# Kernel optimization log

Measured on AMD Instinct MI355X. Metric: run time of the kernel, lower is better.

The kernel has to match this reference:

```python
import jax, jax.numpy as jnp
import numpy as np

EPS = 1e-5


def setup_inputs() -> dict:
    key = jax.random.key(0)
    k1, k2, k3 = jax.random.split(key, 3)
    B, D, T = 16, 256, 4096
    K = 2048
    x = jax.random.normal(k1, (B, D, T), dtype=jnp.float32)
    embedding_sum = jax.random.normal(k2, (K, D), dtype=jnp.float32)
    cluster_usage = jax.random.uniform(k3, (K,), dtype=jnp.float32)
    return {"x": x, "embedding_sum": embedding_sum, "cluster_usage": cluster_usage}


def reference(x, embedding_sum, cluster_usage):
    # embedding property: embedding_sum / clamp(cluster_usage, min=eps)
    emb = embedding_sum / jnp.clip(cluster_usage, EPS, None)[:, None]  # [K, D]
    B, D, T = x.shape
    x_flat = jnp.transpose(x, (0, 2, 1)).reshape(B * T, D)  # (b t) d
    # compute faithfully (clamped for numerical safety).
    x2 = jnp.sum(x_flat * x_flat, axis=-1, keepdims=True)      # [BT, 1]
    e2 = jnp.sum(emb * emb, axis=-1)                           # [K]
    d2 = x2 - 2.0 * (x_flat @ emb.T) + e2[None, :]             # [BT, K]
    distances = jnp.sqrt(jnp.clip(d2, 0.0, None))
    codes = jnp.argmin(distances, axis=-1).reshape(B, 1, T)    # int codes
    # decode: embedding gather, b t d -> b d t
    decoded = jnp.transpose(emb[codes[:, 0, :]], (0, 2, 1))    # [B, D, T]
    return codes, decoded
```

## Files before the change

kernel.cpp:

```cpp
#include <hip/hip_runtime.h>
#include <hip/hip_fp16.h>
#include <cmath>

#define EPS 1e-5f
#define TAU 0.15f
#define RP  8

#define Bn 16
#define Dn 256
#define Tn 4096
#define Kn 2048

typedef unsigned short ushort_t;
typedef __attribute__((ext_vector_type(8))) _Float16 f16x8;
typedef __attribute__((ext_vector_type(4))) float f32x4;

__device__ __forceinline__ unsigned short f2h(float v) {
    return __half_as_ushort(__float2half_rn(v));
}

#define GLOAD_LDS16(gp, lp) __builtin_amdgcn_global_load_lds( \
    (const __attribute__((address_space(1))) unsigned int*)(gp), \
    (__attribute__((address_space(3))) unsigned int*)(lp), 16, 0, 0)

__global__ __launch_bounds__(256) void prep_kernel(
    const float* __restrict__ es, const float* __restrict__ usage,
    float* __restrict__ emb, ushort_t* __restrict__ e16,
    float* __restrict__ bias, float4* __restrict__ embT4,
    int* __restrict__ counter)
{
    __shared__ float sh[256];
    __shared__ float wsum[4];
    const int k = blockIdx.x;
    const int d = threadIdx.x;
    const float inv = 1.0f / fmaxf(usage[k], EPS);
    const float v = es[(size_t)k * Dn + d] * inv;
    emb[(size_t)k * Dn + d] = v;
    e16[(size_t)k * Dn + d] = f2h(fminf(fmaxf(v, -65504.f), 65504.f));
    sh[d] = v;
    float sq = v * v;
    #pragma unroll
    for (int off = 32; off > 0; off >>= 1) sq += __shfl_down(sq, off, 64);
    const int lane = d & 63, wv = d >> 6;
    if (lane == 0) wsum[wv] = sq;
    __syncthreads();
    if (d < 64)
        embT4[(size_t)d * Kn + k] = make_float4(sh[4*d], sh[4*d+1], sh[4*d+2], sh[4*d+3]);
    if (d == 0) {
        bias[k] = 0.5f * (wsum[0] + wsum[1] + wsum[2] + wsum[3]);
        if (k == 0) *counter = 0;
    }
}

__global__ __launch_bounds__(256) void xsplit_kernel(
    const float* __restrict__ x, ushort_t* __restrict__ xh)
{
    __shared__ float tile[32 * 65];
    const int t0 = blockIdx.x * 64;
    const int d0 = blockIdx.y * 32;
    const int b  = blockIdx.z;
    const int tid = threadIdx.x;

    {
        const int dl = tid >> 3, tq = tid & 7;
        const float* src = x + ((size_t)(b * Dn + d0 + dl)) * Tn + t0 + tq * 8;
        const float4 a = *(const float4*)(src);
        const float4 c = *(const float4*)(src + 4);
        float* row = &tile[dl * 65 + tq * 8];
        row[0] = a.x; row[1] = a.y; row[2] = a.z; row[3] = a.w;
        row[4] = c.x; row[5] = c.y; row[6] = c.z; row[7] = c.w;
    }
    __syncthreads();
    {
        const int t_l = tid >> 2, dq = tid & 3;
        unsigned wh[4];
        #pragma unroll
        for (int i = 0; i < 4; ++i) {
            const float a = tile[(dq * 8 + 2 * i) * 65 + t_l];
            const float g = tile[(dq * 8 + 2 * i + 1) * 65 + t_l];
            wh[i] = (unsigned)f2h(a) | ((unsigned)f2h(g) << 16);
        }
        const size_t o = ((size_t)(b * Tn + t0 + t_l)) * Dn + d0 + dq * 8;
        *(uint4*)(xh + o) = make_uint4(wh[0], wh[1], wh[2], wh[3]);
    }
}

#define BARRIER_PIN()                                                         \
    __builtin_amdgcn_s_barrier();                                             \
    __builtin_amdgcn_sched_barrier(0)

#define STAGE_B(dst, kcc, hh)                                                 \
    {                                                                         \
        _Pragma("unroll")                                                     \
        for (int r = 0; r < 4; ++r) {                                         \
            const int c   = r * 512 + tid;                                    \
            const int row = c >> 4;                                           \
            const int col = (((c & 15) ^ (row & 15)) << 3);                   \
            GLOAD_LDS16(e16 + ((size_t)((kcc) * 128 + row)) * Dn + (hh) * 128 + col, \
                        (dst) + ((r * 512 + (wid << 6)) << 3));               \
        }                                                                     \
    }

#define STAGE_A(dst, hh)                                                      \
    {                                                                         \
        _Pragma("unroll")                                                     \
        for (int r = 0; r < 8; ++r) {                                         \
            const int c   = r * 512 + tid;                                    \
            const int row = c >> 4;                                           \
            const int col = (((c & 15) ^ (row & 15)) << 3);                   \
            GLOAD_LDS16(xh + (bTt0 + row) * Dn + (hh) * 128 + col,            \
                        (dst) + ((r * 512 + (wid << 6)) << 3));               \
        }                                                                     \
    }

#define READ_AF(afArr, buf)                                                   \
    {                                                                         \
        _Pragma("unroll")                                                     \
        for (int ks = 0; ks < 4; ++ks)                                        \
            _Pragma("unroll")                                                 \
            for (int i = 0; i < 2; ++i)                                       \
                afArr[ks * 2 + i] = *(const f16x8*)(                          \
                    &(buf)[((wm << 5) + (i << 4) + l15) * 128 +               \
                           ((((ks << 2) | quad) ^ l15) << 3)]);               \
    }

#define COMPUTE_ACC(bbuf, afArr)                                              \
    {                                                                         \
        __builtin_amdgcn_s_setprio(1);                                        \
        _Pragma("unroll")                                                     \
        for (int ks = 0; ks < 4; ++ks)                                        \
            _Pragma("unroll")                                                 \
            for (int j = 0; j < 8; ++j) {                                     \
                const f16x8 bf = *(const f16x8*)(                             \
                    &(bbuf)[((j << 4) + l15) * 128 +                          \
                            ((((ks << 2) | quad) ^ l15) << 3)]);              \
                _Pragma("unroll")                                             \
                for (int i = 0; i < 2; ++i)                                   \
                    acc[i][j] = __builtin_amdgcn_mfma_f32_16x16x32_f16(       \
                        afArr[ks * 2 + i], bf, acc[i][j], 0, 0, 0);           \
            }                                                                 \
        __builtin_amdgcn_s_setprio(0);                                        \
    }

__global__ __launch_bounds__(512, 2) void gemm_argmax(
    const ushort_t* __restrict__ xh, const ushort_t* __restrict__ e16,
    const float* __restrict__ bias_g, int* __restrict__ codes_i,
    float* __restrict__ codes_f, int* __restrict__ list,
    int* __restrict__ counter)
{
    __shared__ __align__(16) ushort_t AsS[256 * 128];
    __shared__ __align__(16) ushort_t BsS[2][128 * 128];
    __shared__ __align__(16) float    biasLds[2048];

    const int bid = blockIdx.x;
    const int b   = bid >> 4;
    const int tt  = bid & 15;
    const int t0  = tt << 8;

    const int tid  = threadIdx.x;
    const int lane = tid & 63;
    const int wid  = tid >> 6;
    const int l15  = lane & 15;
    const int quad = lane >> 4;
    const int wm   = wid;

    const size_t bTt0 = (size_t)b * Tn + t0;

    f16x8 af0[8], af1[8];
    f32x4 acc[2][8];
    float S1[2][4], S2[2][4];
    int   K1[2][4];
    #pragma unroll
    for (int i = 0; i < 2; ++i)
        #pragma unroll
        for (int r = 0; r < 4; ++r) { S1[i][r] = -INFINITY; S2[i][r] = -INFINITY; K1[i][r] = 0; }
    #pragma unroll
    for (int i = 0; i < 2; ++i)
        #pragma unroll
        for (int j = 0; j < 8; ++j)
            acc[i][j] = (f32x4){-INFINITY, -INFINITY, -INFINITY, -INFINITY};

    GLOAD_LDS16(bias_g + (tid << 2), biasLds + (wid << 8));
    STAGE_A(AsS, 0);
    STAGE_A(&BsS[0][0], 1);
    asm volatile("s_waitcnt vmcnt(8)" ::: "memory");
    BARRIER_PIN();
    READ_AF(af0, AsS);
    asm volatile("s_waitcnt vmcnt(0)" ::: "memory");
    BARRIER_PIN();
    READ_AF(af1, (&BsS[0][0]));
    asm volatile("s_waitcnt lgkmcnt(0)" ::: "memory");
    __builtin_amdgcn_sched_barrier(0);
    BARRIER_PIN();
    STAGE_B(&BsS[0][0], 0, 0);
    STAGE_B(&BsS[1][0], 0, 1);

    #pragma unroll 1
    for (int kc = 0; kc < 16; ++kc) {
        asm volatile("s_waitcnt vmcnt(4)" ::: "memory");
        BARRIER_PIN();
        {
            float bj[8];
            #pragma unroll
            for (int j = 0; j < 8; ++j)
                bj[j] = biasLds[(kc << 7) + (j << 4) + l15];
            const int kdrb = ((kc - 1) << 7) + l15;
            __builtin_amdgcn_s_setprio(1);
            #pragma unroll
            for (int j = 0; j < 8; ++j) {
                const f16x8 bf0 = *(const f16x8*)(
                    &BsS[0][((j << 4) + l15) * 128 + ((quad ^ l15) << 3)]);
                const float nb = -bj[j];
                const f32x4 cin = {nb, nb, nb, nb};
                const int kdr = kdrb + (j << 4);
                #pragma unroll
                for (int i = 0; i < 2; ++i) {
                    #pragma unroll
                    for (int r = 0; r < 4; ++r) {
                        const float s = acc[i][j][r];
                        S2[i][r] = __builtin_amdgcn_fmed3f(s, S1[i][r], S2[i][r]);
                        const bool gt = s > S1[i][r];
                        K1[i][r] = gt ? kdr : K1[i][r];
                        S1[i][r] = fmaxf(S1[i][r], s);
                    }
                    acc[i][j] = __builtin_amdgcn_mfma_f32_16x16x32_f16(
                        af0[i], bf0, cin, 0, 0, 0);
                }
            }
            #pragma unroll
            for (int ks = 1; ks < 4; ++ks)
                #pragma unroll
                for (int j = 0; j < 8; ++j) {
                    const f16x8 bf = *(const f16x8*)(
                        &BsS[0][((j << 4) + l15) * 128 +
                                ((((ks << 2) | quad) ^ l15) << 3)]);
                    #pragma unroll
                    for (int i = 0; i < 2; ++i)
                        acc[i][j] = __builtin_amdgcn_mfma_f32_16x16x32_f16(
                            af0[ks * 2 + i], bf, acc[i][j], 0, 0, 0);
                }
            __builtin_amdgcn_s_setprio(0);
        }
        BARRIER_PIN();
        if (kc < 15) STAGE_B(&BsS[0][0], kc + 1, 0);

        if (kc < 15) { asm volatile("s_waitcnt vmcnt(4)" ::: "memory"); }
        else         { asm volatile("s_waitcnt vmcnt(0)" ::: "memory"); }
        BARRIER_PIN();
        COMPUTE_ACC((&BsS[1][0]), af1);
        BARRIER_PIN();
        if (kc < 15) STAGE_B(&BsS[1][0], kc + 1, 1);
    }

    __builtin_amdgcn_sched_barrier(0);

    {
        const int kfb = (15 << 7) + l15;
        #pragma unroll
        for (int j = 0; j < 8; ++j) {
            const int kf = kfb + (j << 4);
            #pragma unroll
            for (int i = 0; i < 2; ++i)
                #pragma unroll
                for (int r = 0; r < 4; ++r) {
                    const float s = acc[i][j][r];
                    S2[i][r] = __builtin_amdgcn_fmed3f(s, S1[i][r], S2[i][r]);
                    const bool gt = s > S1[i][r];
                    K1[i][r] = gt ? kf : K1[i][r];
                    S1[i][r] = fmaxf(S1[i][r], s);
                }
        }
    }

    #pragma unroll
    for (int m = 1; m <= 8; m <<= 1) {
        #pragma unroll
        for (int i = 0; i < 2; ++i)
            #pragma unroll
            for (int r = 0; r < 4; ++r) {
                const float os1 = __shfl_xor(S1[i][r], m);
                const float os2 = __shfl_xor(S2[i][r], m);
                const int   ok1 = __shfl_xor(K1[i][r], m);
                const bool take = (os1 > S1[i][r]) || (os1 == S1[i][r] && ok1 < K1[i][r]);
                const float ns2 = take ? fmaxf(S1[i][r], os2) : fmaxf(S2[i][r], os1);
                if (take) { S1[i][r] = os1; K1[i][r] = ok1; }
                S2[i][r] = ns2;
            }
    }

    if (l15 == 0) {
        #pragma unroll
        for (int i = 0; i < 2; ++i)
            #pragma unroll
            for (int r = 0; r < 4; ++r) {
                const int row = (wm << 5) + (i << 4) + (quad << 2) + r;
                const size_t p = bTt0 + row;
                const int wk = K1[i][r];
                codes_i[p] = wk;
                codes_f[p] = (float)wk;
                if (S1[i][r] - S2[i][r] < TAU) {
                    const int idx = atomicAdd(counter, 1);
                    list[idx] = (int)p;
                }
            }
    }
}

__global__ __launch_bounds__(256) void rescue_kernel(
    const float* __restrict__ x, const float4* __restrict__ embT4,
    const float* __restrict__ bias, const int* __restrict__ list,
    const int* __restrict__ counter, int* __restrict__ codes_i,
    float* __restrict__ codes_f)
{
    __shared__ float xv[RP][256];
    __shared__ int plist[RP];
    __shared__ float rs[RP][4];
    __shared__ int   rk[RP][4];
    const int tid = threadIdx.x, lane = tid & 63, wid = tid >> 6;
    const int count = *counter;
    for (int base = blockIdx.x * RP; base < count; base += gridDim.x * RP) {
        const int npts = min(RP, count - base);
        __syncthreads();
        if (tid < npts) plist[tid] = list[base + tid];
        __syncthreads();
        for (int pi = 0; pi < npts; ++pi) {
            const int p = plist[pi];
            xv[pi][tid] = x[((size_t)((p >> 12) * Dn + tid)) * Tn + (p & 4095)];
        }
        for (int pi = npts; pi < RP; ++pi) xv[pi][tid] = 0.f;
        __syncthreads();

        float acc[8][RP];
        #pragma unroll
        for (int s = 0; s < 8; ++s)
            #pragma unroll
            for (int pi = 0; pi < RP; ++pi) acc[s][pi] = 0.f;

        for (int dc = 0; dc < 64; ++dc) {
            float4 ev[8];
            #pragma unroll
            for (int s = 0; s < 8; ++s)
                ev[s] = embT4[(size_t)dc * Kn + tid + (s << 8)];
            #pragma unroll
            for (int pi = 0; pi < RP; ++pi) {
                const float4 xw = *(const float4*)&xv[pi][dc << 2];
                #pragma unroll
                for (int s = 0; s < 8; ++s)
                    acc[s][pi] += ev[s].x * xw.x + ev[s].y * xw.y
                                + ev[s].z * xw.z + ev[s].w * xw.w;
            }
        }

        float bs[RP]; int bk[RP];
        #pragma unroll
        for (int pi = 0; pi < RP; ++pi) { bs[pi] = -INFINITY; bk[pi] = 0; }
        #pragma unroll
        for (int s = 0; s < 8; ++s) {
            const int kk = tid + (s << 8);
            const float bv = bias[kk];
            #pragma unroll
            for (int pi = 0; pi < RP; ++pi) {
                const float sc = acc[s][pi] - bv;
                if (sc > bs[pi]) { bs[pi] = sc; bk[pi] = kk; }
            }
        }
        #pragma unroll
        for (int off = 1; off < 64; off <<= 1) {
            #pragma unroll
            for (int pi = 0; pi < RP; ++pi) {
                const float os = __shfl_xor(bs[pi], off);
                const int   ok = __shfl_xor(bk[pi], off);
                if (os > bs[pi] || (os == bs[pi] && ok < bk[pi])) { bs[pi] = os; bk[pi] = ok; }
            }
        }
        if (lane == 0) {
            #pragma unroll
            for (int pi = 0; pi < RP; ++pi) { rs[pi][wid] = bs[pi]; rk[pi][wid] = bk[pi]; }
        }
        __syncthreads();
        if (tid < npts) {
            float fs = rs[tid][0]; int fk = rk[tid][0];
            #pragma unroll
            for (int w = 1; w < 4; ++w) {
                if (rs[tid][w] > fs || (rs[tid][w] == fs && rk[tid][w] < fk)) {
                    fs = rs[tid][w]; fk = rk[tid][w];
                }
            }
            const int p = plist[tid];
            codes_i[p] = fk;
            codes_f[p] = (float)fk;
        }
    }
}

__global__ __launch_bounds__(256) void decode_kernel(
    const float* __restrict__ emb, const int* __restrict__ codes,
    float* __restrict__ out)
{
    const int b = blockIdx.y;
    const int t = blockIdx.x * 256 + threadIdx.x;
    const int c = codes[(size_t)b * Tn + t];
    const float4* e4 = (const float4*)(emb + (size_t)c * Dn);
    float* ob = out + (size_t)b * Dn * Tn + t;
    #pragma unroll 4
    for (int d4 = 0; d4 < 64; ++d4) {
        const float4 v = e4[d4];
        ob[(size_t)(d4 * 4 + 0) * Tn] = v.x;
        ob[(size_t)(d4 * 4 + 1) * Tn] = v.y;
        ob[(size_t)(d4 * 4 + 2) * Tn] = v.z;
        ob[(size_t)(d4 * 4 + 3) * Tn] = v.w;
    }
}

extern "C" void kernel_launch(void* const* d_in, const int* in_sizes, int n_in,
                              void* d_out, int out_size, void* d_ws, size_t ws_size,
                              hipStream_t stream) {
    const float* x     = (const float*)d_in[0];
    const float* es    = (const float*)d_in[1];
    const float* usage = (const float*)d_in[2];

    char* ws = (char*)d_ws;
    float*    emb     = (float*)(ws + 0);
    float*    bias    = (float*)(ws + 2097152);
    ushort_t* e16     = (ushort_t*)(ws + 2105344);
    float4*   embT4   = (float4*)(ws + 3153920);
    int*      codes_i = (int*)(ws + 5251072);
    int*      list    = (int*)(ws + 5513216);
    int*      counter = (int*)(ws + 5775360);

    float* codes_f = (float*)d_out;
    float* decoded = (float*)d_out + (size_t)Bn * Tn;

    ushort_t* xh  = (ushort_t*)decoded;

    prep_kernel<<<Kn, 256, 0, stream>>>(es, usage, emb, e16, bias, embT4, counter);

    dim3 gx(Tn / 64, Dn / 32, Bn);
    xsplit_kernel<<<gx, 256, 0, stream>>>(x, xh);

    gemm_argmax<<<256, 512, 0, stream>>>(xh, e16, bias, codes_i, codes_f,
                                         list, counter);

    rescue_kernel<<<1024, 256, 0, stream>>>(x, embT4, bias, list, counter, codes_i, codes_f);

    dim3 g6(Tn / 256, Bn);
    decode_kernel<<<g6, 256, 0, stream>>>(emb, codes_i, decoded);
}
```

Before: 326.8 us.

## Use four-slot LDS ring for B tiles and software-pipeline LDS fragment reads

Replaces the separate A buffer and double-buffered B buffers with a four-slot LDS ring, so B tiles are prefetched one half-step further ahead and each half-iteration needs one barrier instead of two. LDS reads of B fragments are batched per k-step into register arrays and double-buffered, with explicit lgkmcnt waits so MFMAs overlap the next fragment loads. The cost is more registers for the fragment arrays and tighter vmcnt accounting, where a wrong count could cause races.

```diff
diff --git a/kernel.cpp b/kernel.cpp
--- a/kernel.cpp
+++ b/kernel.cpp
@@ -89,6 +89,14 @@
     __builtin_amdgcn_s_barrier();                                             \
     __builtin_amdgcn_sched_barrier(0)
 
+#define LGKM8()                                                               \
+    asm volatile("s_waitcnt lgkmcnt(8)" ::: "memory");                        \
+    __builtin_amdgcn_sched_barrier(0)
+
+#define LGKM0()                                                               \
+    asm volatile("s_waitcnt lgkmcnt(0)" ::: "memory");                        \
+    __builtin_amdgcn_sched_barrier(0)
+
 #define STAGE_B(dst, kcc, hh)                                                 \
     {                                                                         \
         _Pragma("unroll")                                                     \
@@ -124,21 +132,24 @@
                            ((((ks << 2) | quad) ^ l15) << 3)]);               \
     }
 
-#define COMPUTE_ACC(bbuf, afArr)                                              \
+#define READ_BF(dst, bb, ks)                                                  \
+    {                                                                         \
+        _Pragma("unroll")                                                     \
+        for (int j = 0; j < 8; ++j)                                           \
+            dst[j] = *(const f16x8*)((bb) + ((j << 4) + l15) * 128 +          \
+                                     ((((ks << 2) | quad) ^ l15) << 3));      \
+    }
+
+#define MFMA_GRP(afArr, ks, bfArr)                                            \
     {                                                                         \
         __builtin_amdgcn_s_setprio(1);                                        \
         _Pragma("unroll")                                                     \
-        for (int ks = 0; ks < 4; ++ks)                                        \
-            _Pragma("unroll")                                                 \
-            for (int j = 0; j < 8; ++j) {                                     \
-                const f16x8 bf = *(const f16x8*)(                             \
-                    &(bbuf)[((j << 4) + l15) * 128 +                          \
-                            ((((ks << 2) | quad) ^ l15) << 3)]);              \
-                _Pragma("unroll")                                             \
-                for (int i = 0; i < 2; ++i)                                   \
-                    acc[i][j] = __builtin_amdgcn_mfma_f32_16x16x32_f16(       \
-                        afArr[ks * 2 + i], bf, acc[i][j], 0, 0, 0);           \
-            }                                                                 \
+        for (int j = 0; j < 8; ++j) {                                         \
+            acc[0][j] = __builtin_amdgcn_mfma_f32_16x16x32_f16(               \
+                afArr[(ks) * 2], bfArr[j], acc[0][j], 0, 0, 0);               \
+            acc[1][j] = __builtin_amdgcn_mfma_f32_16x16x32_f16(               \
+                afArr[(ks) * 2 + 1], bfArr[j], acc[1][j], 0, 0, 0);           \
+        }                                                                     \
         __builtin_amdgcn_s_setprio(0);                                        \
     }
 
@@ -148,8 +159,7 @@
     float* __restrict__ codes_f, int* __restrict__ list,
     int* __restrict__ counter)
 {
-    __shared__ __align__(16) ushort_t AsS[256 * 128];
-    __shared__ __align__(16) ushort_t BsS[2][128 * 128];
+    __shared__ __align__(16) ushort_t Bring[4][128 * 128];
     __shared__ __align__(16) float    biasLds[2048];
 
     const int bid = blockIdx.x;
@@ -165,6 +175,7 @@
     const int wm   = wid;
 
     const size_t bTt0 = (size_t)b * Tn + t0;
+    ushort_t* const ring = &Bring[0][0];
 
     f16x8 af0[8], af1[8];
     f32x4 acc[2][8];
@@ -181,35 +192,44 @@
             acc[i][j] = (f32x4){-INFINITY, -INFINITY, -INFINITY, -INFINITY};
 
     GLOAD_LDS16(bias_g + (tid << 2), biasLds + (wid << 8));
-    STAGE_A(AsS, 0);
-    STAGE_A(&BsS[0][0], 1);
+    STAGE_A(ring, 0);
+    STAGE_A(ring + (2 << 14), 1);
     asm volatile("s_waitcnt vmcnt(8)" ::: "memory");
     BARRIER_PIN();
-    READ_AF(af0, AsS);
+    READ_AF(af0, ring);
     asm volatile("s_waitcnt vmcnt(0)" ::: "memory");
+    LGKM0();
     BARRIER_PIN();
-    READ_AF(af1, (&BsS[0][0]));
-    asm volatile("s_waitcnt lgkmcnt(0)" ::: "memory");
-    __builtin_amdgcn_sched_barrier(0);
+    READ_AF(af1, (ring + (2 << 14)));
+    LGKM0();
     BARRIER_PIN();
-    STAGE_B(&BsS[0][0], 0, 0);
-    STAGE_B(&BsS[1][0], 0, 1);
+    STAGE_B(ring,             0, 0);
+    STAGE_B(ring + (1 << 14), 0, 1);
+    STAGE_B(ring + (2 << 14), 1, 0);
 
     #pragma unroll 1
     for (int kc = 0; kc < 16; ++kc) {
-        asm volatile("s_waitcnt vmcnt(4)" ::: "memory");
+        ushort_t* const bb0 = ring + ((((kc << 1))     & 3) << 14);
+        ushort_t* const bb1 = ring + ((((kc << 1) + 1) & 3) << 14);
+        ushort_t* const st0 = ring + ((((kc << 1) + 3) & 3) << 14);
+        ushort_t* const st1 = ring + ((((kc << 1) + 4) & 3) << 14);
+        f16x8 bfA[8], bfB[8];
+
+        if (kc < 15) { asm volatile("s_waitcnt vmcnt(8)" ::: "memory"); }
+        else         { asm volatile("s_waitcnt vmcnt(4)" ::: "memory"); }
         BARRIER_PIN();
+        if (kc < 15) STAGE_B(st0, kc + 1, 1);
+        float bj[8];
+        #pragma unroll
+        for (int j = 0; j < 8; ++j) bj[j] = biasLds[(kc << 7) + (j << 4) + l15];
+        READ_BF(bfA, bb0, 0);
+        READ_BF(bfB, bb0, 1);
+        LGKM8();
         {
-            float bj[8];
-            #pragma unroll
-            for (int j = 0; j < 8; ++j)
-                bj[j] = biasLds[(kc << 7) + (j << 4) + l15];
             const int kdrb = ((kc - 1) << 7) + l15;
             __builtin_amdgcn_s_setprio(1);
             #pragma unroll
             for (int j = 0; j < 8; ++j) {
-                const f16x8 bf0 = *(const f16x8*)(
-                    &BsS[0][((j << 4) + l15) * 128 + ((quad ^ l15) << 3)]);
                 const float nb = -bj[j];
                 const f32x4 cin = {nb, nb, nb, nb};
                 const int kdr = kdrb + (j << 4);
@@ -224,32 +244,36 @@
                         S1[i][r] = fmaxf(S1[i][r], s);
                     }
                     acc[i][j] = __builtin_amdgcn_mfma_f32_16x16x32_f16(
-                        af0[i], bf0, cin, 0, 0, 0);
+                        af0[i], bfA[j], cin, 0, 0, 0);
                 }
             }
-            #pragma unroll
-            for (int ks = 1; ks < 4; ++ks)
-                #pragma unroll
-                for (int j = 0; j < 8; ++j) {
-                    const f16x8 bf = *(const f16x8*)(
-                        &BsS[0][((j << 4) + l15) * 128 +
-                                ((((ks << 2) | quad) ^ l15) << 3)]);
-                    #pragma unroll
-                    for (int i = 0; i < 2; ++i)
-                        acc[i][j] = __builtin_amdgcn_mfma_f32_16x16x32_f16(
-                            af0[ks * 2 + i], bf, acc[i][j], 0, 0, 0);
-                }
             __builtin_amdgcn_s_setprio(0);
         }
-        BARRIER_PIN();
-        if (kc < 15) STAGE_B(&BsS[0][0], kc + 1, 0);
-
-        if (kc < 15) { asm volatile("s_waitcnt vmcnt(4)" ::: "memory"); }
+        READ_BF(bfA, bb0, 2);
+        LGKM8();
+        MFMA_GRP(af0, 1, bfB);
+        READ_BF(bfB, bb0, 3);
+        LGKM8();
+        MFMA_GRP(af0, 2, bfA);
+        LGKM0();
+        MFMA_GRP(af0, 3, bfB);
+
+        if (kc < 15) { asm volatile("s_waitcnt vmcnt(8)" ::: "memory"); }
         else         { asm volatile("s_waitcnt vmcnt(0)" ::: "memory"); }
         BARRIER_PIN();
-        COMPUTE_ACC((&BsS[1][0]), af1);
-        BARRIER_PIN();
-        if (kc < 15) STAGE_B(&BsS[1][0], kc + 1, 1);
+        if (kc < 14) STAGE_B(st1, kc + 2, 0);
+        READ_BF(bfA, bb1, 0);
+        READ_BF(bfB, bb1, 1);
+        LGKM8();
+        MFMA_GRP(af1, 0, bfA);
+        READ_BF(bfA, bb1, 2);
+        LGKM8();
+        MFMA_GRP(af1, 1, bfB);
+        READ_BF(bfB, bb1, 3);
+        LGKM8();
+        MFMA_GRP(af1, 2, bfA);
+        LGKM0();
+        MFMA_GRP(af1, 3, bfB);
     }
 
     __builtin_amdgcn_sched_barrier(0);
```

Result: slower. 362.1 us (+10.8%).

## Fuse x transpose/fp16 conversion into GEMM A-fragment loads, drop xsplit kernel

Applied to the files above, without the earlier changes.

Removes the separate xsplit kernel that transposed x into an fp16 (b t d) buffer. The GEMM now loads its A fragments straight from the fp32 [B,D,T] tensor into registers and converts them to half on the fly, and the A staging LDS buffer goes away. This saves one kernel launch and a full write and re-read of the fp16 copy of x. In exchange the loads are strided scalar fp32 reads with per-lane coalescing along T only, which may be less efficient than the old vectorised staged loads.

```diff
diff --git a/kernel.cpp b/kernel.cpp
--- a/kernel.cpp
+++ b/kernel.cpp
@@ -52,39 +52,6 @@
     }
 }
 
-__global__ __launch_bounds__(256) void xsplit_kernel(
-    const float* __restrict__ x, ushort_t* __restrict__ xh)
-{
-    __shared__ float tile[32 * 65];
-    const int t0 = blockIdx.x * 64;
-    const int d0 = blockIdx.y * 32;
-    const int b  = blockIdx.z;
-    const int tid = threadIdx.x;
-
-    {
-        const int dl = tid >> 3, tq = tid & 7;
-        const float* src = x + ((size_t)(b * Dn + d0 + dl)) * Tn + t0 + tq * 8;
-        const float4 a = *(const float4*)(src);
-        const float4 c = *(const float4*)(src + 4);
-        float* row = &tile[dl * 65 + tq * 8];
-        row[0] = a.x; row[1] = a.y; row[2] = a.z; row[3] = a.w;
-        row[4] = c.x; row[5] = c.y; row[6] = c.z; row[7] = c.w;
-    }
-    __syncthreads();
-    {
-        const int t_l = tid >> 2, dq = tid & 3;
-        unsigned wh[4];
-        #pragma unroll
-        for (int i = 0; i < 4; ++i) {
-            const float a = tile[(dq * 8 + 2 * i) * 65 + t_l];
-            const float g = tile[(dq * 8 + 2 * i + 1) * 65 + t_l];
-            wh[i] = (unsigned)f2h(a) | ((unsigned)f2h(g) << 16);
-        }
-        const size_t o = ((size_t)(b * Tn + t0 + t_l)) * Dn + d0 + dq * 8;
-        *(uint4*)(xh + o) = make_uint4(wh[0], wh[1], wh[2], wh[3]);
-    }
-}
-
 #define BARRIER_PIN()                                                         \
     __builtin_amdgcn_s_barrier();                                             \
     __builtin_amdgcn_sched_barrier(0)
@@ -99,29 +66,6 @@
             GLOAD_LDS16(e16 + ((size_t)((kcc) * 128 + row)) * Dn + (hh) * 128 + col, \
                         (dst) + ((r * 512 + (wid << 6)) << 3));               \
         }                                                                     \
-    }
-
-#define STAGE_A(dst, hh)                                                      \
-    {                                                                         \
-        _Pragma("unroll")                                                     \
-        for (int r = 0; r < 8; ++r) {                                         \
-            const int c   = r * 512 + tid;                                    \
-            const int row = c >> 4;                                           \
-            const int col = (((c & 15) ^ (row & 15)) << 3);                   \
-            GLOAD_LDS16(xh + (bTt0 + row) * Dn + (hh) * 128 + col,            \
-                        (dst) + ((r * 512 + (wid << 6)) << 3));               \
-        }                                                                     \
-    }
-
-#define READ_AF(afArr, buf)                                                   \
-    {                                                                         \
-        _Pragma("unroll")                                                     \
-        for (int ks = 0; ks < 4; ++ks)                                        \
-            _Pragma("unroll")                                                 \
-            for (int i = 0; i < 2; ++i)                                       \
-                afArr[ks * 2 + i] = *(const f16x8*)(                          \
-                    &(buf)[((wm << 5) + (i << 4) + l15) * 128 +               \
-                           ((((ks << 2) | quad) ^ l15) << 3)]);               \
     }
 
 #define COMPUTE_ACC(bbuf, afArr)                                              \
@@ -143,12 +87,11 @@
     }
 
 __global__ __launch_bounds__(512, 2) void gemm_argmax(
-    const ushort_t* __restrict__ xh, const ushort_t* __restrict__ e16,
+    const float* __restrict__ x, const ushort_t* __restrict__ e16,
     const float* __restrict__ bias_g, int* __restrict__ codes_i,
     float* __restrict__ codes_f, int* __restrict__ list,
     int* __restrict__ counter)
 {
-    __shared__ __align__(16) ushort_t AsS[256 * 128];
     __shared__ __align__(16) ushort_t BsS[2][128 * 128];
     __shared__ __align__(16) float    biasLds[2048];
 
@@ -166,7 +109,29 @@
 
     const size_t bTt0 = (size_t)b * Tn + t0;
 
+    GLOAD_LDS16(bias_g + (tid << 2), biasLds + (wid << 8));
+
     f16x8 af0[8], af1[8];
+    {
+        const float* xb = x + (size_t)b * Dn * Tn;
+        #pragma unroll
+        for (int ks = 0; ks < 4; ++ks)
+            #pragma unroll
+            for (int i = 0; i < 2; ++i) {
+                const int t = t0 + (wm << 5) + (i << 4) + l15;
+                const float* c0 = xb + ((size_t)(ks * 32 + quad * 8)) * Tn + t;
+                const float* c1 = c0 + (size_t)128 * Tn;
+                f16x8 v0, v1;
+                #pragma unroll
+                for (int e = 0; e < 8; ++e) {
+                    v0[e] = (_Float16)c0[(size_t)e * Tn];
+                    v1[e] = (_Float16)c1[(size_t)e * Tn];
+                }
+                af0[ks * 2 + i] = v0;
+                af1[ks * 2 + i] = v1;
+            }
+    }
+
     f32x4 acc[2][8];
     float S1[2][4], S2[2][4];
     int   K1[2][4];
@@ -180,17 +145,7 @@
         for (int j = 0; j < 8; ++j)
             acc[i][j] = (f32x4){-INFINITY, -INFINITY, -INFINITY, -INFINITY};
 
-    GLOAD_LDS16(bias_g + (tid << 2), biasLds + (wid << 8));
-    STAGE_A(AsS, 0);
-    STAGE_A(&BsS[0][0], 1);
-    asm volatile("s_waitcnt vmcnt(8)" ::: "memory");
-    BARRIER_PIN();
-    READ_AF(af0, AsS);
     asm volatile("s_waitcnt vmcnt(0)" ::: "memory");
-    BARRIER_PIN();
-    READ_AF(af1, (&BsS[0][0]));
-    asm volatile("s_waitcnt lgkmcnt(0)" ::: "memory");
-    __builtin_amdgcn_sched_barrier(0);
     BARRIER_PIN();
     STAGE_B(&BsS[0][0], 0, 0);
     STAGE_B(&BsS[1][0], 0, 1);
@@ -431,14 +386,9 @@
     float* codes_f = (float*)d_out;
     float* decoded = (float*)d_out + (size_t)Bn * Tn;
 
-    ushort_t* xh  = (ushort_t*)decoded;
-
     prep_kernel<<<Kn, 256, 0, stream>>>(es, usage, emb, e16, bias, embT4, counter);
 
-    dim3 gx(Tn / 64, Dn / 32, Bn);
-    xsplit_kernel<<<gx, 256, 0, stream>>>(x, xh);
-
-    gemm_argmax<<<256, 512, 0, stream>>>(xh, e16, bias, codes_i, codes_f,
+    gemm_argmax<<<256, 512, 0, stream>>>(x, e16, bias, codes_i, codes_f,
                                          list, counter);
 
     rescue_kernel<<<1024, 256, 0, stream>>>(x, embT4, bias, list, counter, codes_i, codes_f);
```

Result: faster. 306.0 us (-6.4%).
